# Kernel optimization log

Hardware: AMD Instinct MI355X
Metric: run time of the kernel (lower is better)

The kernel has to match this reference:

```python
import jax, jax.numpy as jnp
import numpy as np

B, L, D, H = 4, 1024, 1024, 16
HD = D // H            # head_dim = 64
MAX_LEN = 1024         # pos_max_len
SCALE = HD ** 0.5


def setup_inputs() -> dict:
    key = jax.random.key(0)
    ks = jax.random.split(key, 7)
    sd = 1.0 / np.sqrt(D)
    x = jax.random.normal(ks[0], (B, L, D), dtype=jnp.float32)
    Wq = jax.random.normal(ks[1], (D, D), dtype=jnp.float32) * sd
    Wk = jax.random.normal(ks[2], (D, D), dtype=jnp.float32) * sd
    Wv = jax.random.normal(ks[3], (D, D), dtype=jnp.float32) * sd
    Wo = jax.random.normal(ks[4], (D, D), dtype=jnp.float32) * sd
    # relative positional embedding tables [2*max_len+1, head_dim]
    pek = jax.random.normal(ks[5], (2 * MAX_LEN + 1, HD), dtype=jnp.float32) / np.sqrt(HD)
    pev = jax.random.normal(ks[6], (2 * MAX_LEN + 1, HD), dtype=jnp.float32) / np.sqrt(HD)
    return {"x": x, "Wq": Wq, "Wk": Wk, "Wv": Wv, "Wo": Wo, "pek": pek, "pev": pev}


def _rel_idx(seq_len):
    r = jnp.arange(seq_len)
    dist = r[None, :] - r[:, None]                 # k - q, [L, L]
    return jnp.clip(dist, -MAX_LEN, MAX_LEN) + MAX_LEN


def reference(x, Wq, Wk, Wv, Wo, pek, pev):
    b, s, _ = x.shape
    # projections (nn.Linear: x @ W.T), split heads -> [b, h, s, d]
    def proj(W):
        return (x @ W.T).reshape(b, s, H, HD).transpose(0, 2, 1, 3)
    Q, K, V = proj(Wq), proj(Wk), proj(Wv)

    scores = jnp.einsum('bhqd,bhkd->bhqk', Q, K) / SCALE
    idx = _rel_idx(s)                              # [s, s]
    rel_k = pek[idx]                               # [s, s, hd]
    scores = scores + jnp.einsum('bhqd,qkd->bhqk', Q, rel_k) / SCALE

    causal = jnp.tril(jnp.ones((s, s), dtype=bool))
    scores = jnp.where(causal[None, None], scores, -jnp.inf)
    attn = jax.nn.softmax(scores, axis=-1)         # [b, h, q, k]

    out = jnp.einsum('bhqk,bhkd->bhqd', attn, V)
    rel_v = pev[idx]                               # [s, s, hd]
    out = out + jnp.einsum('bhqk,qkd->bhqd', attn, rel_v)

    out = out.transpose(0, 2, 1, 3).reshape(b, s, D)
    return out @ Wo.T
```

## Files before the change

kernel.cpp:

```cpp
#include <hip/hip_runtime.h>
#include <hip/hip_bf16.h>

typedef __hip_bfloat16 bf16;
using bfv8 = __attribute__((ext_vector_type(8))) __bf16;
using f4_t = __attribute__((ext_vector_type(4))) float;

#define DEVI static __device__ __forceinline__

DEVI unsigned short f2bu(float f) {
    bf16 h = __float2bfloat16(f);
    return __builtin_bit_cast(unsigned short, h);
}
DEVI ushort4 f4_to_b4(float4 v) {
    ushort4 r;
    r.x = f2bu(v.x); r.y = f2bu(v.y); r.z = f2bu(v.z); r.w = f2bu(v.w);
    return r;
}
DEVI void gl2lds16(const void* g, void* l) {
    __builtin_amdgcn_global_load_lds((const __attribute__((address_space(1))) void*)g,
                                     (__attribute__((address_space(3))) void*)l, 16, 0, 0);
}

template<int N>
DEVI float row_ror(float x) {
    return __builtin_bit_cast(float,
        __builtin_amdgcn_update_dpp(0, __builtin_bit_cast(int, x), 0x120 | N, 0xF, 0xF, false));
}
DEVI float max16(float x) {
    x = fmaxf(x, row_ror<8>(x));
    x = fmaxf(x, row_ror<4>(x));
    x = fmaxf(x, row_ror<2>(x));
    x = fmaxf(x, row_ror<1>(x));
    return x;
}
DEVI float sum16(float x) {
    x += row_ror<8>(x);
    x += row_ror<4>(x);
    x += row_ror<2>(x);
    x += row_ror<1>(x);
    return x;
}

__global__ __launch_bounds__(256) void prep_cast(
    const float* __restrict__ x, const float* __restrict__ wq, const float* __restrict__ wk,
    const float* __restrict__ wv, const float* __restrict__ wo,
    bf16* __restrict__ xb, bf16* __restrict__ wqb, bf16* __restrict__ wkb,
    bf16* __restrict__ wvb, bf16* __restrict__ wob)
{
    size_t i = (size_t)blockIdx.x * 256 + threadIdx.x;
    const size_t X4 = 1u << 20, W4 = 1u << 18;
    const float* src; bf16* dst; size_t off;
    if (i < X4)              { src = x;  dst = xb;  off = i; }
    else if (i < X4 + W4)    { src = wq; dst = wqb; off = i - X4; }
    else if (i < X4 + 2*W4)  { src = wk; dst = wkb; off = i - X4 - W4; }
    else if (i < X4 + 3*W4)  { src = wv; dst = wvb; off = i - X4 - 2*W4; }
    else                     { src = wo; dst = wob; off = i - X4 - 3*W4; }
    float4 v = ((const float4*)src)[off];
    ((ushort4*)dst)[off] = f4_to_b4(v);
}

__global__ __launch_bounds__(256) void prep_blocks(
    const float* __restrict__ pek, const float* __restrict__ pev,
    bf16* __restrict__ pekBlk, bf16* __restrict__ pevBlk)
{
    __shared__ bf16 t[64][72];
    const int b = blockIdx.x;
    const int r = threadIdx.x >> 2, c0 = (threadIdx.x & 3) * 16;

    if (b < 17) {
        const float* src = pek + (size_t)(64 * b + 1 + r) * 64 + c0;
        bf16* dst = pekBlk + (size_t)b * 4096 + r * 64 + c0;
#pragma unroll
        for (int j = 0; j < 16; j += 4)
            *(ushort4*)(dst + j) = f4_to_b4(*(const float4*)(src + j));
    }
    {
        const float* src = pev + (size_t)(64 * b + 1 + r) * 64 + c0;
#pragma unroll
        for (int j = 0; j < 16; j++) t[r][c0 + j] = __float2bfloat16(src[j]);
        __syncthreads();
        bf16* dst = pevBlk + (size_t)b * 4096 + r * 64 + c0;
#pragma unroll
        for (int j = 0; j < 16; j++) dst[j] = t[c0 + j][r];
    }
}

__global__ __launch_bounds__(256, 4) void gemm_bt3(
    const bf16* __restrict__ A,
    const bf16* __restrict__ B0, const bf16* __restrict__ B1, const bf16* __restrict__ B2,
    bf16* __restrict__ outb, bf16* __restrict__ vtb, float* __restrict__ outf,
    int K, int mode)
{
    __shared__ __align__(16) bf16 smem[64 * 64 + 128 * 64];
    bf16* As = smem;
    bf16* Bs = smem + 64 * 64;
    bf16* Cb = smem;

    const int tid  = threadIdx.x;
    const int lane = tid & 63, wave = tid >> 6;
    const int quad = lane >> 4, l16 = lane & 15;
    const int wr = wave >> 1, wc = wave & 1;
    const int m0 = blockIdx.y * 64, n0 = blockIdx.x * 128;
    const int z = blockIdx.z;
    const bf16* Bm = (z == 0) ? B0 : (z == 1) ? B1 : B2;

    f4_t zero = {0.f, 0.f, 0.f, 0.f};
    f4_t acc[2][4];
#pragma unroll
    for (int i = 0; i < 2; i++)
#pragma unroll
        for (int j = 0; j < 4; j++) acc[i][j] = zero;

    const int srow8 = lane >> 3;
    const int scol  = (lane & 7) * 8;
    const bf16* Ag = A  + (size_t)(m0 + 16 * wave + srow8) * K + scol;
    const bf16* Bg = Bm + (size_t)(n0 + 32 * wave + srow8) * K + scol;

    for (int k0 = 0; k0 < K; k0 += 64) {
#pragma unroll
        for (int i = 0; i < 2; i++)
            gl2lds16(Ag + (size_t)(8 * i) * K + k0, &As[(16 * wave + 8 * i) * 64]);
#pragma unroll
        for (int i = 0; i < 4; i++)
            gl2lds16(Bg + (size_t)(8 * i) * K + k0, &Bs[(32 * wave + 8 * i) * 64]);
        __syncthreads();
#pragma unroll
        for (int ks = 0; ks < 2; ks++) {
            bfv8 af[2], bfr[4];
#pragma unroll
            for (int mt = 0; mt < 2; mt++)
                af[mt] = *(const bfv8*)&As[(wr * 32 + mt * 16 + l16) * 64 + ks * 32 + quad * 8];
#pragma unroll
            for (int nt = 0; nt < 4; nt++)
                bfr[nt] = *(const bfv8*)&Bs[(wc * 64 + nt * 16 + l16) * 64 + ks * 32 + quad * 8];
#pragma unroll
            for (int mt = 0; mt < 2; mt++)
#pragma unroll
                for (int nt = 0; nt < 4; nt++)
                    acc[mt][nt] = __builtin_amdgcn_mfma_f32_16x16x32_bf16(af[mt], bfr[nt], acc[mt][nt], 0, 0, 0);
        }
        __syncthreads();
    }

    if (mode == 1) {
#pragma unroll
        for (int mt = 0; mt < 2; mt++)
#pragma unroll
            for (int nt = 0; nt < 4; nt++)
#pragma unroll
                for (int r = 0; r < 4; r++) {
                    int m = m0 + wr * 32 + mt * 16 + quad * 4 + r;
                    int n = n0 + wc * 64 + nt * 16 + l16;
                    outf[(size_t)m * 1024 + n] = acc[mt][nt][r];
                }
        return;
    }

    const int b  = m0 >> 10, l0 = m0 & 1023, h0 = n0 >> 6;
    if (z < 2) {
#pragma unroll
        for (int mt = 0; mt < 2; mt++)
#pragma unroll
            for (int nt = 0; nt < 4; nt++)
#pragma unroll
                for (int r = 0; r < 4; r++) {
                    int mm = wr * 32 + mt * 16 + quad * 4 + r;
                    int nn = wc * 64 + nt * 16 + l16;
                    Cb[mm * 136 + nn] = __float2bfloat16(acc[mt][nt][r]);
                }
        __syncthreads();
        bf16* ob = outb + (size_t)z * (4 * 16 * 1024 * 64);
        const int ri = tid >> 1, hp = ri >> 6, lrow = ri & 63, c0 = (tid & 1) * 32;
        bf16* dst = ob + ((size_t)((b * 16 + h0 + hp) * 1024) + l0 + lrow) * 64 + c0;
        const bf16* srcl = &Cb[lrow * 136 + hp * 64 + c0];
#pragma unroll
        for (int j = 0; j < 4; j++)
            *(int4*)(dst + 8 * j) = *(const int4*)(srcl + 8 * j);
    } else {
#pragma unroll
        for (int mt = 0; mt < 2; mt++)
#pragma unroll
            for (int nt = 0; nt < 4; nt++)
#pragma unroll
                for (int r = 0; r < 4; r++) {
                    int mm = wr * 32 + mt * 16 + quad * 4 + r;
                    int nn = wc * 64 + nt * 16 + l16;
                    Cb[nn * 72 + mm] = __float2bfloat16(acc[mt][nt][r]);
                }
        __syncthreads();
        const int ri = tid >> 1, c0 = (tid & 1) * 32;
        const int n = n0 + ri, h = n >> 6, hd = n & 63;
        bf16* dst = vtb + ((size_t)((b * 16 + h) * 64 + hd)) * 1024 + l0 + c0;
        const bf16* srcl = &Cb[ri * 72 + c0];
#pragma unroll
        for (int j = 0; j < 4; j++)
            *(int4*)(dst + 8 * j) = *(const int4*)(srcl + 8 * j);
    }
}

__global__ __launch_bounds__(256, 2) void attn_k(
    const bf16* __restrict__ Qb, const bf16* __restrict__ Kb, const bf16* __restrict__ Vtb,
    const bf16* __restrict__ pekBlk, const bf16* __restrict__ pevBlk, bf16* __restrict__ Ob)
{
    constexpr int ST = 104;
    __shared__ __align__(16) bf16 Ks[64 * 64];
    __shared__ __align__(16) bf16 Vs[64 * 64];
    __shared__ __align__(16) bf16 pekR[2 * 4096];
    __shared__ __align__(16) bf16 pevR[3 * 4096];
    __shared__ __align__(16) bf16 sU[4][16 * ST];
    __shared__ __align__(16) bf16 sP[4][16 * 72];

    const int tid  = threadIdx.x;
    const int lane = tid & 63, wave = tid >> 6;
    const int quad = lane >> 4, l16 = lane & 15;
    const int bh = blockIdx.x;
    const int g  = 15 - blockIdx.y;
    const int s  = 4 * g + wave;
    const int nkt = g + 1;

    bf16* myU = sU[wave];
    bf16* myP = sP[wave];

    const int srow8 = lane >> 3;
    const int scg   = (lane & 7) ^ srow8;
    const int x8    = l16 & 7;

    {
        int* p = (int*)myU;
#pragma unroll
        for (int i = 0; i < 13; i++) p[lane + 64 * i] = 0;
    }

    bfv8 qf[2];
    {
        const bf16* qp = Qb + ((size_t)bh * 1024 + 16 * s + l16) * 64 + quad * 8;
        qf[0] = *(const bfv8*)qp;
        qf[1] = *(const bfv8*)(qp + 32);
#pragma unroll
        for (int j = 0; j < 8; j++) {
            qf[0][j] = (__bf16)((float)qf[0][j] * 0.125f);
            qf[1][j] = (__bf16)((float)qf[1][j] * 0.125f);
        }
    }

    f4_t zero = {0.f, 0.f, 0.f, 0.f};
    f4_t o_acc[4];
    float m_i[4], l_i[4];
#pragma unroll
    for (int i = 0; i < 4; i++) { o_acc[i] = zero; m_i[i] = -1e30f; l_i[i] = 0.f; }

    const bf16* Kbh = Kb  + (size_t)bh * 1024 * 64;
    const bf16* Vbh = Vtb + (size_t)bh * 64 * 1024;
    const int B0 = 15 - g;

#pragma unroll
    for (int i = 0; i < 2; i++) {
        const int row = 8 * wave + 32 * i + srow8;
        gl2lds16(Kbh + (size_t)row * 64 + scg * 8, &Ks[(8 * wave + 32 * i) * 64]);
        gl2lds16(Vbh + (size_t)row * 1024 + scg * 8, &Vs[(8 * wave + 32 * i) * 64]);
    }
#pragma unroll
    for (int i2 = 0; i2 < 2; i2++) {
        const int slot = (B0 + i2) & 1;
#pragma unroll
        for (int i = 0; i < 2; i++) {
            const int row = 16 * wave + 8 * i + srow8;
            gl2lds16(pekBlk + (size_t)(B0 + i2) * 4096 + row * 64 + scg * 8,
                     &pekR[slot * 4096 + (16 * wave + 8 * i) * 64]);
        }
    }
#pragma unroll
    for (int i2 = 0; i2 < 3; i2++) {
        const int slot = (B0 + i2) % 3;
#pragma unroll
        for (int i = 0; i < 2; i++) {
            const int row = 16 * wave + 8 * i + srow8;
            gl2lds16(pevBlk + (size_t)(B0 + i2) * 4096 + row * 64 + scg * 8,
                     &pevR[slot * 4096 + (16 * wave + 8 * i) * 64]);
        }
    }
    __syncthreads();

    bfv8 stK[2], stV[2], stPk[2], stPv[2];

    for (int kt = 0; kt < nkt; kt++) {
        const int k0 = kt << 6;
        const int Bb = kt - g + 15;
        const int bm3 = Bb % 3;
        const bool pf = (kt + 1 < nkt);

        if (pf) {
            const int k0n = (kt + 1) << 6;
            const int bNew = Bb + 2, cNew = Bb + 3;
#pragma unroll
            for (int i = 0; i < 2; i++) {
                const int row = 8 * wave + 32 * i + srow8;
                stK[i] = *(const bfv8*)(Kbh + (size_t)(k0n + row) * 64 + scg * 8);
                stV[i] = *(const bfv8*)(Vbh + (size_t)row * 1024 + k0n + scg * 8);
            }
#pragma unroll
            for (int i = 0; i < 2; i++) {
                const int row = 16 * wave + 8 * i + srow8;
                stPk[i] = *(const bfv8*)(pekBlk + (size_t)bNew * 4096 + row * 64 + scg * 8);
                stPv[i] = *(const bfv8*)(pevBlk + (size_t)cNew * 4096 + row * 64 + scg * 8);
            }
        }

        f4_t s1[4], tt[5];
#pragma unroll
        for (int i = 0; i < 4; i++) s1[i] = zero;
#pragma unroll
        for (int i = 0; i < 5; i++) tt[i] = zero;
#pragma unroll
        for (int ks = 0; ks < 2; ks++) {
#pragma unroll
            for (int nt = 0; nt < 4; nt++) {
                bfv8 kf = *(const bfv8*)&Ks[(nt * 16 + l16) * 64 + ((ks * 4 + quad) ^ x8) * 8];
                s1[nt] = __builtin_amdgcn_mfma_f32_16x16x32_bf16(qf[ks], kf, s1[nt], 0, 0, 0);
            }
#pragma unroll
            for (int nt = 0; nt < 5; nt++) {
                const int off  = 48 - 16 * wave + 16 * nt;
                const int slot = (Bb + (off >> 6)) & 1;
                bfv8 pfr = *(const bfv8*)&pekR[slot * 4096 + ((off & 63) + l16) * 64
                                              + ((ks * 4 + quad) ^ x8) * 8];
                tt[nt] = __builtin_amdgcn_mfma_f32_16x16x32_bf16(qf[ks], pfr, tt[nt], 0, 0, 0);
            }
        }

        float sc[4][4];
#pragma unroll
        for (int r = 0; r < 4; r++) {
            int qq = quad * 4 + r;
            int t  = l16 + 15 - qq;
            int srcl = quad * 16 + (t & 15);
            bool lo = (t < 16);
            float rot[5];
#pragma unroll
            for (int j = 0; j < 5; j++) rot[j] = __shfl(tt[j][r], srcl, 64);
#pragma unroll
            for (int nt = 0; nt < 4; nt++) {
                float s2 = lo ? rot[nt] : rot[nt + 1];
                float v = s1[nt][r] + s2;
                int kk = nt * 16 + l16;
                if (k0 + kk > 16 * s + qq) v = -1e30f;
                sc[nt][r] = v;
            }
        }

        float alpha[4];
#pragma unroll
        for (int r = 0; r < 4; r++) {
            float mt = fmaxf(fmaxf(sc[0][r], sc[1][r]), fmaxf(sc[2][r], sc[3][r]));
            mt = max16(mt);
            float mnew = fmaxf(m_i[r], mt);
            alpha[r] = __expf(m_i[r] - mnew);
            m_i[r] = mnew;
        }
#pragma unroll
        for (int nt = 0; nt < 4; nt++)
#pragma unroll
            for (int r = 0; r < 4; r++)
                sc[nt][r] = __expf(sc[nt][r] - m_i[r]);
#pragma unroll
        for (int r = 0; r < 4; r++) {
            float rs = sum16(sc[0][r] + sc[1][r] + sc[2][r] + sc[3][r]);
            l_i[r] = l_i[r] * alpha[r] + rs;
#pragma unroll
            for (int nt = 0; nt < 4; nt++) o_acc[nt][r] *= alpha[r];
        }

#pragma unroll
        for (int nt = 0; nt < 4; nt++)
#pragma unroll
            for (int r = 0; r < 4; r++) {
                int qq = quad * 4 + r;
                int kk = nt * 16 + l16;
                bf16 pb = __float2bfloat16(sc[nt][r]);
                myP[qq * 72 + kk] = pb;
                myU[qq * ST + kk - qq + 15] = pb;
            }

#pragma unroll
        for (int ks = 0; ks < 2; ks++) {
            bfv8 pa = *(const bfv8*)&myP[l16 * 72 + ks * 32 + quad * 8];
#pragma unroll
            for (int nt = 0; nt < 4; nt++) {
                bfv8 vf = *(const bfv8*)&Vs[(nt * 16 + l16) * 64 + ((ks * 4 + quad) ^ x8) * 8];
                o_acc[nt] = __builtin_amdgcn_mfma_f32_16x16x32_bf16(pa, vf, o_acc[nt], 0, 0, 0);
            }
        }
#pragma unroll
        for (int ks = 0; ks < 3; ks++) {
            bfv8 ua = *(const bfv8*)&myU[l16 * ST + ks * 32 + quad * 8];
            const int off2 = 48 - 16 * wave + 32 * ks + 8 * quad;
            int slot2 = bm3 + (off2 >> 6);
            if (slot2 >= 3) slot2 -= 3;
            const int chunk = (((off2 & 63) >> 3) ^ x8);
#pragma unroll
            for (int nt = 0; nt < 4; nt++) {
                bfv8 pvf = *(const bfv8*)&pevR[slot2 * 4096 + (nt * 16 + l16) * 64 + chunk * 8];
                o_acc[nt] = __builtin_amdgcn_mfma_f32_16x16x32_bf16(ua, pvf, o_acc[nt], 0, 0, 0);
            }
        }
        __syncthreads();

        if (pf) {
            const int Bn = Bb + 1;
            const int slotK = (Bn + 1) & 1, slotV = (Bn + 2) % 3;
#pragma unroll
            for (int i = 0; i < 2; i++) {
                *(bfv8*)&Ks[(8 * wave + 32 * i) * 64 + lane * 8] = stK[i];
                *(bfv8*)&Vs[(8 * wave + 32 * i) * 64 + lane * 8] = stV[i];
            }
#pragma unroll
            for (int i = 0; i < 2; i++) {
                *(bfv8*)&pekR[slotK * 4096 + (16 * wave + 8 * i) * 64 + lane * 8] = stPk[i];
                *(bfv8*)&pevR[slotV * 4096 + (16 * wave + 8 * i) * 64 + lane * 8] = stPv[i];
            }
        }
        __syncthreads();
    }

    const int b = bh >> 4, h = bh & 15;
#pragma unroll
    for (int nt = 0; nt < 4; nt++)
#pragma unroll
        for (int r = 0; r < 4; r++) {
            int q = 16 * s + quad * 4 + r;
            int d = nt * 16 + l16;
            Ob[((size_t)(b * 1024 + q)) * 1024 + h * 64 + d] = __float2bfloat16(o_acc[nt][r] / l_i[r]);
        }
}

extern "C" void kernel_launch(void* const* d_in, const int* in_sizes, int n_in,
                              void* d_out, int out_size, void* d_ws, size_t ws_size,
                              hipStream_t stream) {
    const float* x   = (const float*)d_in[0];
    const float* Wq  = (const float*)d_in[1];
    const float* Wk  = (const float*)d_in[2];
    const float* Wv  = (const float*)d_in[3];
    const float* Wo  = (const float*)d_in[4];
    const float* pek = (const float*)d_in[5];
    const float* pev = (const float*)d_in[6];

    const size_t MB = 1u << 20;
    char* ws = (char*)d_ws;
    bf16* xb     = (bf16*)(ws + 0);
    bf16* Wqb    = (bf16*)(ws + 8  * MB);
    bf16* Wkb    = (bf16*)(ws + 10 * MB);
    bf16* Wvb    = (bf16*)(ws + 12 * MB);
    bf16* Wob    = (bf16*)(ws + 14 * MB);
    bf16* Qb     = (bf16*)(ws + 16 * MB);
    bf16* Kb     = (bf16*)(ws + 24 * MB);
    bf16* Vtb    = (bf16*)(ws + 32 * MB);
    bf16* pekBlk = (bf16*)(ws + 48 * MB);
    bf16* pevBlk = (bf16*)(ws + 48 * MB + 256*1024);
    bf16* Ao     = xb;

    prep_cast<<<dim3(8192), 256, 0, stream>>>(x, Wq, Wk, Wv, Wo, xb, Wqb, Wkb, Wvb, Wob);
    prep_blocks<<<dim3(18), 256, 0, stream>>>(pek, pev, pekBlk, pevBlk);
    gemm_bt3<<<dim3(8, 64, 3), 256, 0, stream>>>(xb, Wqb, Wkb, Wvb, Qb, Vtb, nullptr, 1024, 0);
    attn_k<<<dim3(64, 16), 256, 0, stream>>>(Qb, Kb, Vtb, pekBlk, pevBlk, Ao);
    gemm_bt3<<<dim3(8, 64, 1), 256, 0, stream>>>(Ao, Wob, nullptr, nullptr, nullptr, nullptr, (float*)d_out, 1024, 1);
}
```

Baseline: 225.8 us.

## Stream pev fragments from global into registers to free LDS for occupancy

Drops the triple-buffered pev tile from LDS and instead loads the pev B-fragments for the rel-V MFMA straight from global memory into registers, issued before the softmax so the latency can overlap that work. The P staging buffer moves to a 64-element stride with an XOR swizzle to avoid bank conflicts, which also trims LDS. Launch bounds go from 2 to 3 blocks per CU to use the freed LDS. The costs are more global/L2 traffic per tile, loads that are less fully hidden, and tighter register limits that may cause spills with 12 extra vector fragments live.

```diff
diff --git a/kernel.cpp b/kernel.cpp
--- a/kernel.cpp
+++ b/kernel.cpp
@@ -198,7 +198,7 @@
     }
 }
 
-__global__ __launch_bounds__(256, 2) void attn_k(
+__global__ __launch_bounds__(256, 3) void attn_k(
     const bf16* __restrict__ Qb, const bf16* __restrict__ Kb, const bf16* __restrict__ Vtb,
     const bf16* __restrict__ pekBlk, const bf16* __restrict__ pevBlk, bf16* __restrict__ Ob)
 {
@@ -206,9 +206,8 @@
     __shared__ __align__(16) bf16 Ks[64 * 64];
     __shared__ __align__(16) bf16 Vs[64 * 64];
     __shared__ __align__(16) bf16 pekR[2 * 4096];
-    __shared__ __align__(16) bf16 pevR[3 * 4096];
     __shared__ __align__(16) bf16 sU[4][16 * ST];
-    __shared__ __align__(16) bf16 sP[4][16 * 72];
+    __shared__ __align__(16) bf16 sP[4][16 * 64];
 
     const int tid  = threadIdx.x;
     const int lane = tid & 63, wave = tid >> 6;
@@ -269,29 +268,18 @@
                      &pekR[slot * 4096 + (16 * wave + 8 * i) * 64]);
         }
     }
-#pragma unroll
-    for (int i2 = 0; i2 < 3; i2++) {
-        const int slot = (B0 + i2) % 3;
-#pragma unroll
-        for (int i = 0; i < 2; i++) {
-            const int row = 16 * wave + 8 * i + srow8;
-            gl2lds16(pevBlk + (size_t)(B0 + i2) * 4096 + row * 64 + scg * 8,
-                     &pevR[slot * 4096 + (16 * wave + 8 * i) * 64]);
-        }
-    }
     __syncthreads();
 
-    bfv8 stK[2], stV[2], stPk[2], stPv[2];
+    bfv8 stK[2], stV[2], stPk[2];
 
     for (int kt = 0; kt < nkt; kt++) {
         const int k0 = kt << 6;
         const int Bb = kt - g + 15;
-        const int bm3 = Bb % 3;
         const bool pf = (kt + 1 < nkt);
 
         if (pf) {
             const int k0n = (kt + 1) << 6;
-            const int bNew = Bb + 2, cNew = Bb + 3;
+            const int bNew = Bb + 2;
 #pragma unroll
             for (int i = 0; i < 2; i++) {
                 const int row = 8 * wave + 32 * i + srow8;
@@ -302,7 +290,6 @@
             for (int i = 0; i < 2; i++) {
                 const int row = 16 * wave + 8 * i + srow8;
                 stPk[i] = *(const bfv8*)(pekBlk + (size_t)bNew * 4096 + row * 64 + scg * 8);
-                stPv[i] = *(const bfv8*)(pevBlk + (size_t)cNew * 4096 + row * 64 + scg * 8);
             }
         }
 
@@ -348,6 +335,16 @@
             }
         }
 
+        bfv8 pvf[3][4];
+#pragma unroll
+        for (int ks = 0; ks < 3; ks++) {
+            const int t0 = Bb * 64 + 48 - 16 * wave + 32 * ks + 8 * quad;
+            const bf16* pvW = pevBlk + (size_t)(t0 >> 6) * 4096 + (t0 & 63);
+#pragma unroll
+            for (int nt = 0; nt < 4; nt++)
+                pvf[ks][nt] = *(const bfv8*)(pvW + (size_t)(nt * 16 + l16) * 64);
+        }
+
         float alpha[4];
 #pragma unroll
         for (int r = 0; r < 4; r++) {
@@ -377,13 +374,13 @@
                 int qq = quad * 4 + r;
                 int kk = nt * 16 + l16;
                 bf16 pb = __float2bfloat16(sc[nt][r]);
-                myP[qq * 72 + kk] = pb;
+                myP[qq * 64 + (((kk >> 3) ^ (qq & 7)) << 3) + (kk & 7)] = pb;
                 myU[qq * ST + kk - qq + 15] = pb;
             }
 
 #pragma unroll
         for (int ks = 0; ks < 2; ks++) {
-            bfv8 pa = *(const bfv8*)&myP[l16 * 72 + ks * 32 + quad * 8];
+            bfv8 pa = *(const bfv8*)&myP[l16 * 64 + (((ks * 4 + quad) ^ x8) << 3)];
 #pragma unroll
             for (int nt = 0; nt < 4; nt++) {
                 bfv8 vf = *(const bfv8*)&Vs[(nt * 16 + l16) * 64 + ((ks * 4 + quad) ^ x8) * 8];
@@ -393,31 +390,23 @@
 #pragma unroll
         for (int ks = 0; ks < 3; ks++) {
             bfv8 ua = *(const bfv8*)&myU[l16 * ST + ks * 32 + quad * 8];
-            const int off2 = 48 - 16 * wave + 32 * ks + 8 * quad;
-            int slot2 = bm3 + (off2 >> 6);
-            if (slot2 >= 3) slot2 -= 3;
-            const int chunk = (((off2 & 63) >> 3) ^ x8);
-#pragma unroll
-            for (int nt = 0; nt < 4; nt++) {
-                bfv8 pvf = *(const bfv8*)&pevR[slot2 * 4096 + (nt * 16 + l16) * 64 + chunk * 8];
-                o_acc[nt] = __builtin_amdgcn_mfma_f32_16x16x32_bf16(ua, pvf, o_acc[nt], 0, 0, 0);
-            }
+#pragma unroll
+            for (int nt = 0; nt < 4; nt++)
+                o_acc[nt] = __builtin_amdgcn_mfma_f32_16x16x32_bf16(ua, pvf[ks][nt], o_acc[nt], 0, 0, 0);
         }
         __syncthreads();
 
         if (pf) {
             const int Bn = Bb + 1;
-            const int slotK = (Bn + 1) & 1, slotV = (Bn + 2) % 3;
+            const int slotK = (Bn + 1) & 1;
 #pragma unroll
             for (int i = 0; i < 2; i++) {
                 *(bfv8*)&Ks[(8 * wave + 32 * i) * 64 + lane * 8] = stK[i];
                 *(bfv8*)&Vs[(8 * wave + 32 * i) * 64 + lane * 8] = stV[i];
             }
 #pragma unroll
-            for (int i = 0; i < 2; i++) {
+            for (int i = 0; i < 2; i++)
                 *(bfv8*)&pekR[slotK * 4096 + (16 * wave + 8 * i) * 64 + lane * 8] = stPk[i];
-                *(bfv8*)&pevR[slotV * 4096 + (16 * wave + 8 * i) * 64 + lane * 8] = stPv[i];
-            }
         }
         __syncthreads();
     }
```

Result: slower. 341.9 us (+51.4%).

## Enlarge GEMM tile to 128x128 and XOR-swizzle LDS operand layout

Applied to the files above, without the earlier changes.

The projection and output GEMMs now use 128x128 block tiles instead of 64x128, so each wave computes a 64x64 sub-tile with a 4x4 MFMA accumulator array. This halves the grid rows and raises operand reuse per LDS load. The global-to-LDS copy and the fragment reads now XOR-swizzle the 16-byte column groups by row to cut LDS bank conflicts. In exchange, occupancy drops to 2 blocks per SM, the grid has fewer blocks (768 for QKV, 256 for the output GEMM), and more registers are used per thread.

```diff
diff --git a/kernel.cpp b/kernel.cpp
--- a/kernel.cpp
+++ b/kernel.cpp
@@ -85,56 +85,57 @@
     }
 }
 
-__global__ __launch_bounds__(256, 4) void gemm_bt3(
+__global__ __launch_bounds__(256, 2) void gemm_bt4(
     const bf16* __restrict__ A,
     const bf16* __restrict__ B0, const bf16* __restrict__ B1, const bf16* __restrict__ B2,
     bf16* __restrict__ outb, bf16* __restrict__ vtb, float* __restrict__ outf,
     int K, int mode)
 {
-    __shared__ __align__(16) bf16 smem[64 * 64 + 128 * 64];
+    __shared__ __align__(16) bf16 smem[128 * 132];
     bf16* As = smem;
-    bf16* Bs = smem + 64 * 64;
+    bf16* Bs = smem + 128 * 64;
     bf16* Cb = smem;
 
     const int tid  = threadIdx.x;
     const int lane = tid & 63, wave = tid >> 6;
     const int quad = lane >> 4, l16 = lane & 15;
-    const int wr = wave >> 1, wc = wave & 1;
-    const int m0 = blockIdx.y * 64, n0 = blockIdx.x * 128;
+    const int wm = wave >> 1, wn = wave & 1;
+    const int m0 = blockIdx.y * 128, n0 = blockIdx.x * 128;
     const int z = blockIdx.z;
     const bf16* Bm = (z == 0) ? B0 : (z == 1) ? B1 : B2;
 
+    const int srow8 = lane >> 3;
+    const int scg   = (lane & 7) ^ srow8;
+    const int x8    = l16 & 7;
+
     f4_t zero = {0.f, 0.f, 0.f, 0.f};
-    f4_t acc[2][4];
-#pragma unroll
-    for (int i = 0; i < 2; i++)
+    f4_t acc[4][4];
+#pragma unroll
+    for (int i = 0; i < 4; i++)
 #pragma unroll
         for (int j = 0; j < 4; j++) acc[i][j] = zero;
 
-    const int srow8 = lane >> 3;
-    const int scol  = (lane & 7) * 8;
-    const bf16* Ag = A  + (size_t)(m0 + 16 * wave + srow8) * K + scol;
-    const bf16* Bg = Bm + (size_t)(n0 + 32 * wave + srow8) * K + scol;
+    const bf16* Ag = A  + (size_t)(m0 + 32 * wave + srow8) * K + scg * 8;
+    const bf16* Bg = Bm + (size_t)(n0 + 32 * wave + srow8) * K + scg * 8;
 
     for (int k0 = 0; k0 < K; k0 += 64) {
 #pragma unroll
-        for (int i = 0; i < 2; i++)
-            gl2lds16(Ag + (size_t)(8 * i) * K + k0, &As[(16 * wave + 8 * i) * 64]);
-#pragma unroll
-        for (int i = 0; i < 4; i++)
+        for (int i = 0; i < 4; i++) {
+            gl2lds16(Ag + (size_t)(8 * i) * K + k0, &As[(32 * wave + 8 * i) * 64]);
             gl2lds16(Bg + (size_t)(8 * i) * K + k0, &Bs[(32 * wave + 8 * i) * 64]);
+        }
         __syncthreads();
 #pragma unroll
         for (int ks = 0; ks < 2; ks++) {
-            bfv8 af[2], bfr[4];
-#pragma unroll
-            for (int mt = 0; mt < 2; mt++)
-                af[mt] = *(const bfv8*)&As[(wr * 32 + mt * 16 + l16) * 64 + ks * 32 + quad * 8];
+            bfv8 af[4], bfr[4];
+#pragma unroll
+            for (int mt = 0; mt < 4; mt++)
+                af[mt] = *(const bfv8*)&As[(wm * 64 + mt * 16 + l16) * 64 + ((ks * 4 + quad) ^ x8) * 8];
 #pragma unroll
             for (int nt = 0; nt < 4; nt++)
-                bfr[nt] = *(const bfv8*)&Bs[(wc * 64 + nt * 16 + l16) * 64 + ks * 32 + quad * 8];
-#pragma unroll
-            for (int mt = 0; mt < 2; mt++)
+                bfr[nt] = *(const bfv8*)&Bs[(wn * 64 + nt * 16 + l16) * 64 + ((ks * 4 + quad) ^ x8) * 8];
+#pragma unroll
+            for (int mt = 0; mt < 4; mt++)
 #pragma unroll
                 for (int nt = 0; nt < 4; nt++)
                     acc[mt][nt] = __builtin_amdgcn_mfma_f32_16x16x32_bf16(af[mt], bfr[nt], acc[mt][nt], 0, 0, 0);
@@ -144,13 +145,13 @@
 
     if (mode == 1) {
 #pragma unroll
-        for (int mt = 0; mt < 2; mt++)
+        for (int mt = 0; mt < 4; mt++)
 #pragma unroll
             for (int nt = 0; nt < 4; nt++)
 #pragma unroll
                 for (int r = 0; r < 4; r++) {
-                    int m = m0 + wr * 32 + mt * 16 + quad * 4 + r;
-                    int n = n0 + wc * 64 + nt * 16 + l16;
+                    int m = m0 + wm * 64 + mt * 16 + quad * 4 + r;
+                    int n = n0 + wn * 64 + nt * 16 + l16;
                     outf[(size_t)m * 1024 + n] = acc[mt][nt][r];
                 }
         return;
@@ -159,41 +160,41 @@
     const int b  = m0 >> 10, l0 = m0 & 1023, h0 = n0 >> 6;
     if (z < 2) {
 #pragma unroll
-        for (int mt = 0; mt < 2; mt++)
+        for (int mt = 0; mt < 4; mt++)
 #pragma unroll
             for (int nt = 0; nt < 4; nt++)
 #pragma unroll
                 for (int r = 0; r < 4; r++) {
-                    int mm = wr * 32 + mt * 16 + quad * 4 + r;
-                    int nn = wc * 64 + nt * 16 + l16;
-                    Cb[mm * 136 + nn] = __float2bfloat16(acc[mt][nt][r]);
+                    int mm = wm * 64 + mt * 16 + quad * 4 + r;
+                    int nn = wn * 64 + nt * 16 + l16;
+                    Cb[mm * 132 + nn] = __float2bfloat16(acc[mt][nt][r]);
                 }
         __syncthreads();
         bf16* ob = outb + (size_t)z * (4 * 16 * 1024 * 64);
-        const int ri = tid >> 1, hp = ri >> 6, lrow = ri & 63, c0 = (tid & 1) * 32;
-        bf16* dst = ob + ((size_t)((b * 16 + h0 + hp) * 1024) + l0 + lrow) * 64 + c0;
-        const bf16* srcl = &Cb[lrow * 136 + hp * 64 + c0];
-#pragma unroll
-        for (int j = 0; j < 4; j++)
+        const int hp = tid >> 7, lrow = tid & 127;
+        bf16* dst = ob + ((size_t)((b * 16 + h0 + hp) * 1024) + l0 + lrow) * 64;
+        const bf16* srcl = &Cb[lrow * 132 + hp * 64];
+#pragma unroll
+        for (int j = 0; j < 8; j++)
             *(int4*)(dst + 8 * j) = *(const int4*)(srcl + 8 * j);
     } else {
 #pragma unroll
-        for (int mt = 0; mt < 2; mt++)
+        for (int mt = 0; mt < 4; mt++)
 #pragma unroll
             for (int nt = 0; nt < 4; nt++)
 #pragma unroll
                 for (int r = 0; r < 4; r++) {
-                    int mm = wr * 32 + mt * 16 + quad * 4 + r;
-                    int nn = wc * 64 + nt * 16 + l16;
-                    Cb[nn * 72 + mm] = __float2bfloat16(acc[mt][nt][r]);
+                    int mm = wm * 64 + mt * 16 + quad * 4 + r;
+                    int nn = wn * 64 + nt * 16 + l16;
+                    Cb[nn * 132 + mm] = __float2bfloat16(acc[mt][nt][r]);
                 }
         __syncthreads();
-        const int ri = tid >> 1, c0 = (tid & 1) * 32;
+        const int ri = tid >> 1, c0 = (tid & 1) * 64;
         const int n = n0 + ri, h = n >> 6, hd = n & 63;
         bf16* dst = vtb + ((size_t)((b * 16 + h) * 64 + hd)) * 1024 + l0 + c0;
-        const bf16* srcl = &Cb[ri * 72 + c0];
-#pragma unroll
-        for (int j = 0; j < 4; j++)
+        const bf16* srcl = &Cb[ri * 132 + c0];
+#pragma unroll
+        for (int j = 0; j < 8; j++)
             *(int4*)(dst + 8 * j) = *(const int4*)(srcl + 8 * j);
     }
 }
@@ -460,7 +461,7 @@
 
     prep_cast<<<dim3(8192), 256, 0, stream>>>(x, Wq, Wk, Wv, Wo, xb, Wqb, Wkb, Wvb, Wob);
     prep_blocks<<<dim3(18), 256, 0, stream>>>(pek, pev, pekBlk, pevBlk);
-    gemm_bt3<<<dim3(8, 64, 3), 256, 0, stream>>>(xb, Wqb, Wkb, Wvb, Qb, Vtb, nullptr, 1024, 0);
+    gemm_bt4<<<dim3(8, 32, 3), 256, 0, stream>>>(xb, Wqb, Wkb, Wvb, Qb, Vtb, nullptr, 1024, 0);
     attn_k<<<dim3(64, 16), 256, 0, stream>>>(Qb, Kb, Vtb, pekBlk, pevBlk, Ao);
-    gemm_bt3<<<dim3(8, 64, 1), 256, 0, stream>>>(Ao, Wob, nullptr, nullptr, nullptr, nullptr, (float*)d_out, 1024, 1);
-}
+    gemm_bt4<<<dim3(8, 32, 1), 256, 0, stream>>>(Ao, Wob, nullptr, nullptr, nullptr, nullptr, (float*)d_out, 1024, 1);
+}
```

New measurement: 206.3 us. -8.6%, faster.
